# Optimization experiments

Hardware: AMD Instinct MI355X
Metric: run time of the kernel (lower is better)

## Reference

```python
import jax, jax.numpy as jnp
import numpy as np

IN_F = 4096
OUT_F = 4096
R_BLOCKS = 4
D = IN_F // R_BLOCKS          # 1024 block size
NUM_TASKS = 5
POOL = 5
EPS0 = 1e-05
SEQ = 4096


def setup_inputs() -> dict:
    key = jax.random.key(0)
    k1, k2, k3, k4 = jax.random.split(key, 4)
    return {
        "input": jax.random.normal(k1, (1, SEQ, IN_F), jnp.float32),
        "lora_route": jax.random.normal(k2, (NUM_TASKS, IN_F, POOL), jnp.float32) * 0.02,
        "lora_down": jax.random.normal(k3, (NUM_TASKS, R_BLOCKS, D, D), jnp.float32) * 0.01,
        "W": jax.random.normal(k4, (OUT_F, IN_F), jnp.float32) * 0.02,
        "task_id": 5,
    }


def _block_diag(Q):
    # Q: [r, d, d] -> [r*d, r*d] block-diagonal
    r, d, _ = Q.shape
    out = jnp.zeros((r * d, r * d), Q.dtype)
    for i in range(r):
        out = out.at[i * d:(i + 1) * d, i * d:(i + 1) * d].set(Q[i])
    return out


def reference(input, lora_route, lora_down, W, task_id):
    # eval-mode forward of OFTInjectedLinear (block_share=False, is_coft=True)
    n_tasks, in_f, pool = lora_route.shape
    r, d = lora_down.shape[1], lora_down.shape[2]
    # project_batch: eps = (eps0 * d * d) / sqrt(r)
    eps = jnp.asarray(EPS0 * d * d, input.dtype) / jnp.sqrt(jnp.asarray(r, input.dtype))

    route = lora_route[task_id - 1][None]                     # [1, in, pool]
    input_mean = jnp.mean(input, axis=1, keepdims=True)       # [1, 1, in]
    omegas = jax.nn.softmax(jnp.matmul(input_mean, route), axis=2)  # [1, 1, pool]
    omegas_mean = jnp.mean(omegas, axis=(0, 1))[:task_id]     # [task_id]
    k = min(task_id, 2)
    _, I_idx = jax.lax.top_k(omegas_mean, k)                  # selected tasks

    eye_d = jnp.eye(d, dtype=input.dtype)
    delta = jnp.eye(in_f, dtype=input.dtype)
    for i in range(k):                                        # k is a small static int
        j = I_idx[i]
        R = jnp.take(lora_down, j, axis=0)                    # [r, d, d]
        # COFT projection toward the ZERO matrix (source uses torch.zeros for I)
        nrm = jnp.sqrt(jnp.sum(R * R, axis=(1, 2), keepdims=True))  # per-block fro norm
        Rp = jnp.where(nrm <= eps, R, eps * R / jnp.maximum(nrm, 1e-12))
        # batched Cayley: Q = (I - skew) (I + skew)^{-1}
        skew = 0.5 * (Rp - jnp.swapaxes(Rp, 1, 2))
        Q = jnp.matmul(eye_d - skew, jnp.linalg.inv(eye_d + skew))  # [r, d, d]
        bd = _block_diag(Q)                                   # [in, in]
        omega_j = omegas[0, 0, j]                             # scalar (B==1)
        delta = delta * (omega_j * bd)                        # ELEMENTWISE, as in source

    filt = jnp.matmul(delta, W.T)                             # [in, out]
    return jnp.matmul(input, filt)                            # [1, S, out]
```

## Files before the change

kernel.cpp:

```cpp
#include <hip/hip_runtime.h>
#include <stdint.h>


typedef __bf16 bf16;
typedef __bf16 bf16x4 __attribute__((ext_vector_type(4)));
typedef __bf16 bf16x8 __attribute__((ext_vector_type(8)));
typedef float  f32x4  __attribute__((ext_vector_type(4)));

#define AS1 __attribute__((address_space(1)))
#define AS3 __attribute__((address_space(3)))

constexpr size_t OFF_INBF = 0;
constexpr size_t OFF_WV   = OFF_INBF + (size_t)4096 * 4096 * 2;
constexpr size_t OFF_MEAN = OFF_WV + (size_t)4096 * 4096 * 2;
constexpr size_t OFF_INFO = OFF_MEAN + 4096 * 4;
constexpr size_t OFF_V    = OFF_INFO + 64;
constexpr size_t TP_ELEMS  = (size_t)16 * 8192;
constexpr size_t OFF_MPART = OFF_WV + (size_t)1024 * 1024;

__global__ void mean_cvt(const float4* __restrict__ in4, float* __restrict__ mpart,
                         bf16* __restrict__ ob) {
    const int t  = threadIdx.x;
    const int f4 = blockIdx.x * 256 + t;
    const int by = blockIdx.y;
    const int s0 = by * 32;
    float sx = 0.f, sy = 0.f, sz = 0.f, sw = 0.f;
    for (int s = s0; s < s0 + 32; ++s) {
        float4 vx = in4[(size_t)s * 1024 + f4];
        sx += vx.x; sy += vx.y; sz += vx.z; sw += vx.w;
        bf16x4 bv;
        bv[0] = (bf16)vx.x; bv[1] = (bf16)vx.y; bv[2] = (bf16)vx.z; bv[3] = (bf16)vx.w;
        *(bf16x4*)&ob[(size_t)s * 4096 + f4 * 4] = bv;
    }
    float4* mp = (float4*)&mpart[(size_t)by * 4096 + f4 * 4];
    *mp = make_float4(sx, sy, sz, sw);
}

__global__ void omega_kernel(const float* __restrict__ mpart, const float* __restrict__ lora_route,
                             const int* __restrict__ task_id_p, int* __restrict__ info_i,
                             float* __restrict__ info_f) {
    __shared__ float wpart[16][5];
    const int t = threadIdx.x;
    const int tid = task_id_p[0];
    const float* route = lora_route + (size_t)(tid - 1) * 4096 * 5;
    float acc[5] = {0.f, 0.f, 0.f, 0.f, 0.f};
#pragma unroll
    for (int ff = 0; ff < 4; ++ff) {
        const int f = ff * 1024 + t;
        float cs = 0.f;
        for (int by = 0; by < 128; ++by) cs += mpart[(size_t)by * 4096 + f];
        const float m = cs * (1.0f / 4096.0f);
#pragma unroll
        for (int p = 0; p < 5; ++p) acc[p] += m * route[f * 5 + p];
    }
#pragma unroll
    for (int p = 0; p < 5; ++p)
        for (int off = 32; off > 0; off >>= 1) acc[p] += __shfl_xor(acc[p], off);
    if ((t & 63) == 0) {
#pragma unroll
        for (int p = 0; p < 5; ++p) wpart[t >> 6][p] = acc[p];
    }
    __syncthreads();
    if (t == 0) {
        float logits[5];
        for (int p = 0; p < 5; ++p) {
            float s = 0.f;
            for (int ww = 0; ww < 16; ++ww) s += wpart[ww][p];
            logits[p] = s;
        }
        float mx = logits[0];
        for (int p = 1; p < 5; ++p) mx = fmaxf(mx, logits[p]);
        float e[5], se = 0.f;
        for (int p = 0; p < 5; ++p) { e[p] = expf(logits[p] - mx); se += e[p]; }
        float om[5];
        for (int p = 0; p < 5; ++p) om[p] = e[p] / se;
        const int n = tid < 5 ? tid : 5;
        int j1 = 0;
        for (int p = 1; p < n; ++p) if (om[p] > om[j1]) j1 = p;
        int j2 = -1;
        for (int p = 0; p < n; ++p) if (p != j1 && (j2 < 0 || om[p] > om[j2])) j2 = p;
        const int k = tid < 2 ? tid : 2;
        info_i[0] = j1;
        info_i[1] = (k > 1) ? j2 : j1;
        info_i[2] = k;
        float c = om[j1];
        if (k > 1) c *= om[j2];
        info_f[3] = c;
    }
}

__global__ void diag_kernel(const float* __restrict__ lora_down, const int* __restrict__ info_i,
                            float* __restrict__ TP, float* __restrict__ NP) {
    const int bid = blockIdx.x;
    const int ts = bid >> 10;
    const int rb = (bid >> 8) & 3;
    const int a  = (bid >> 4) & 15;
    const int b  = bid & 15;
    const int k = info_i[2];
    if (ts >= k) return;
    const int j = info_i[ts];
    const float* R = lora_down + ((size_t)(j * 4 + rb) << 20);
    __shared__ float X[64][65];
    __shared__ float Y[64][65];
    __shared__ float wsum[4];
    const int t = threadIdx.x;
    const int i = t >> 2, g = t & 3;
    const int a64 = a * 64, b64 = b * 64;
    float nacc = 0.f;
#pragma unroll
    for (int qq = 0; qq < 4; ++qq) {
        const int fi = qq * 256 + t;
        const int row = fi >> 4, c4 = fi & 15;
        float4 vx = *(const float4*)&R[(size_t)(a64 + row) * 1024 + b64 + c4 * 4];
        X[row][c4 * 4 + 0] = vx.x; X[row][c4 * 4 + 1] = vx.y;
        X[row][c4 * 4 + 2] = vx.z; X[row][c4 * 4 + 3] = vx.w;
        nacc += vx.x * vx.x + vx.y * vx.y + vx.z * vx.z + vx.w * vx.w;
        float4 vy = *(const float4*)&R[(size_t)(b64 + row) * 1024 + a64 + c4 * 4];
        Y[row][c4 * 4 + 0] = vy.x; Y[row][c4 * 4 + 1] = vy.y;
        Y[row][c4 * 4 + 2] = vy.z; Y[row][c4 * 4 + 3] = vy.w;
    }
    __syncthreads();
    float tacc = 0.f;
#pragma unroll
    for (int s = 0; s < 16; ++s) {
        float d = X[i][g * 16 + s] - Y[g * 16 + s][i];
        tacc += d * d;
    }
    tacc += __shfl_xor(tacc, 1);
    tacc += __shfl_xor(tacc, 2);
    if (g == 0) TP[b * 8192 + ((ts * 4 + rb) << 10) + a64 + i] = tacc;
    for (int off = 32; off > 0; off >>= 1) nacc += __shfl_down(nacc, off);
    if ((t & 63) == 0) wsum[t >> 6] = nacc;
    __syncthreads();
    if (t == 0) NP[(ts * 4 + rb) * 256 + a * 16 + b] = wsum[0] + wsum[1] + wsum[2] + wsum[3];
}

__global__ void vbuild(const float* __restrict__ TP, const float* __restrict__ NP,
                       const int* __restrict__ info_i, const float* __restrict__ info_f,
                       float* __restrict__ v) {
    __shared__ float red[256];
    __shared__ float snrm[8];
    const int t = threadIdx.x;
    for (int g = 0; g < 8; ++g) {
        red[t] = NP[g * 256 + t];
        __syncthreads();
        for (int s = 128; s > 0; s >>= 1) {
            if (t < s) red[t] += red[t + s];
            __syncthreads();
        }
        if (t == 0) snrm[g] = red[0];
        __syncthreads();
    }
    const int i = blockIdx.x * 256 + t;
    const int k = info_i[2];
    const float c = info_f[3];
    const int rb = i >> 10, di = i & 1023;
    const float eps = 1e-5f * 1024.0f * 1024.0f / 2.0f;
    float q = c;
    for (int ts = 0; ts < k; ++ts) {
        float tt = 0.f;
#pragma unroll
        for (int bb = 0; bb < 16; ++bb) tt += TP[bb * 8192 + ((ts * 4 + rb) << 10) + di];
        float nrm = sqrtf(snrm[ts * 4 + rb]);
        float scale = (nrm <= eps) ? 1.0f : eps / fmaxf(nrm, 1e-12f);
        q *= 1.0f - 0.5f * scale * scale * tt;
    }
    v[i] = q;
}

__global__ void scaleW(const float4* __restrict__ W4, const float* __restrict__ v,
                       bf16* __restrict__ Wv) {
    const size_t stride = (size_t)gridDim.x * blockDim.x;
    for (size_t i = (size_t)blockIdx.x * blockDim.x + threadIdx.x; i < (size_t)4096 * 1024; i += stride) {
        float4 w = W4[i];
        const float* vp = &v[(i & 1023) << 2];
        bf16x4 o;
        o[0] = (bf16)(w.x * vp[0]);
        o[1] = (bf16)(w.y * vp[1]);
        o[2] = (bf16)(w.z * vp[2]);
        o[3] = (bf16)(w.w * vp[3]);
        *(bf16x4*)&Wv[i << 2] = o;
    }
}

__device__ __forceinline__ void gload_lds16(const bf16* g, bf16* lds) {
    __builtin_amdgcn_global_load_lds((const AS1 void*)g, (AS3 void*)lds, 16, 0, 0);
}

__global__ __launch_bounds__(512, 2) void gemm256(const bf16* __restrict__ A,
                                                  const bf16* __restrict__ B,
                                                  float* __restrict__ C) {
    __shared__ bf16 lds[65536];
    const int t = threadIdx.x;
    const int w = t >> 6, l = t & 63;
    const int bid = blockIdx.x;
    const int swz = ((bid & 7) << 5) | (bid >> 3);
    const int bm = swz >> 4, bn = swz & 15;
    const int wm = w >> 2, wn = w & 3;
    const int rl = l & 15, q = l >> 4;
    const int xm = (l & 7) << 4;

    const int srow = (w << 4) + (l >> 3);
    const int scol = ((l & 7) ^ (l >> 3)) << 3;
    const bf16* pA = A + (size_t)((bm << 8) + srow) * 4096 + scol;
    const bf16* pB = B + (size_t)((bn << 8) + srow) * 4096 + scol;

#define STG(dstE, srcP, h, kt) do {                                                          \
        gload_lds16((srcP) + (size_t)((h) * 128) * 4096 + (size_t)(kt) * 64,                 \
                    (bf16*)&lds[(dstE) + (h) * 8192 + w * 1024]);                            \
        gload_lds16((srcP) + (size_t)((h) * 128 + 8) * 4096 + (size_t)(kt) * 64,             \
                    (bf16*)&lds[(dstE) + (h) * 8192 + w * 1024 + 512]);                      \
    } while (0)

    const int aB = (((wm << 7) + rl) << 6);
    const int bB = 16384 + (((wn << 6) + rl) << 6);
    const int c0 = (((q << 4) + 0) ^ xm) >> 1;
    const int c1 = (((q << 4) + 64) ^ xm) >> 1;

    f32x4 acc[8][4] = {};
    bf16x8 a0L[4], a0H[4], a1L[4], a1H[4], b0[4], b1[4], a0n[4];

    STG(0, pA, 0, 0); STG(0, pA, 1, 0);
    STG(16384, pB, 0, 0); STG(16384, pB, 1, 0);
    STG(32768, pA, 0, 1); STG(32768, pA, 1, 1);
    asm volatile("s_waitcnt vmcnt(8)" ::: "memory");
    __builtin_amdgcn_s_barrier();
    asm volatile("" ::: "memory");
#pragma unroll
    for (int m = 0; m < 4; ++m) a0L[m] = *(const bf16x8*)&lds[0 + aB + m * 1024 + c0];

    for (int kt = 0; kt < 64; ++kt) {
        const int cur = (kt & 1) << 15;
        const int nxt = cur ^ 32768;
        if (kt < 63) asm volatile("s_waitcnt vmcnt(4)" ::: "memory");
        else         asm volatile("s_waitcnt vmcnt(0)" ::: "memory");
        __builtin_amdgcn_s_barrier();
        asm volatile("" ::: "memory");

#pragma unroll
        for (int n = 0; n < 4; ++n) b0[n] = *(const bf16x8*)&lds[cur + bB + n * 1024 + c0];
#pragma unroll
        for (int m = 0; m < 4; ++m) a0H[m] = *(const bf16x8*)&lds[cur + aB + (m + 4) * 1024 + c0];
        if (kt + 1 < 64) STG(nxt + 16384, pB, 0, kt + 1);
        __builtin_amdgcn_s_setprio(1);
#pragma unroll
        for (int m = 0; m < 4; ++m)
#pragma unroll
            for (int n = 0; n < 4; ++n)
                acc[m][n] = __builtin_amdgcn_mfma_f32_16x16x32_bf16(a0L[m], b0[n], acc[m][n], 0, 0, 0);
        __builtin_amdgcn_s_setprio(0);
        __builtin_amdgcn_s_barrier();

#pragma unroll
        for (int m = 0; m < 4; ++m) a1L[m] = *(const bf16x8*)&lds[cur + aB + m * 1024 + c1];
#pragma unroll
        for (int n = 0; n < 4; ++n) b1[n] = *(const bf16x8*)&lds[cur + bB + n * 1024 + c1];
        if (kt + 1 < 64) STG(nxt + 16384, pB, 1, kt + 1);
        __builtin_amdgcn_s_setprio(1);
#pragma unroll
        for (int m = 0; m < 4; ++m)
#pragma unroll
            for (int n = 0; n < 4; ++n)
                acc[m + 4][n] = __builtin_amdgcn_mfma_f32_16x16x32_bf16(a0H[m], b0[n], acc[m + 4][n], 0, 0, 0);
        __builtin_amdgcn_s_setprio(0);
        __builtin_amdgcn_s_barrier();

#pragma unroll
        for (int m = 0; m < 4; ++m) a1H[m] = *(const bf16x8*)&lds[cur + aB + (m + 4) * 1024 + c1];
        __builtin_amdgcn_s_setprio(1);
#pragma unroll
        for (int m = 0; m < 4; ++m)
#pragma unroll
            for (int n = 0; n < 4; ++n)
                acc[m][n] = __builtin_amdgcn_mfma_f32_16x16x32_bf16(a1L[m], b1[n], acc[m][n], 0, 0, 0);
        __builtin_amdgcn_s_setprio(0);
        asm volatile("s_waitcnt lgkmcnt(0)" ::: "memory");
        if (kt < 63) asm volatile("s_waitcnt vmcnt(4)" ::: "memory");
        __builtin_amdgcn_s_barrier();
        asm volatile("" ::: "memory");

        if (kt + 2 < 64) { STG(cur, pA, 0, kt + 2); STG(cur, pA, 1, kt + 2); }
        if (kt + 1 < 64) {
#pragma unroll
            for (int m = 0; m < 4; ++m) a0n[m] = *(const bf16x8*)&lds[nxt + aB + m * 1024 + c0];
        }
        __builtin_amdgcn_s_setprio(1);
#pragma unroll
        for (int m = 0; m < 4; ++m)
#pragma unroll
            for (int n = 0; n < 4; ++n)
                acc[m + 4][n] = __builtin_amdgcn_mfma_f32_16x16x32_bf16(a1H[m], b1[n], acc[m + 4][n], 0, 0, 0);
        __builtin_amdgcn_s_setprio(0);
        if (kt + 1 < 64) {
#pragma unroll
            for (int m = 0; m < 4; ++m) a0L[m] = a0n[m];
        }
    }
#undef STG

    const int crow = (bm << 8) + (wm << 7) + (q << 2);
    const int ccol = (bn << 8) + (wn << 6) + rl;
#pragma unroll
    for (int m = 0; m < 8; ++m)
#pragma unroll
        for (int n = 0; n < 4; ++n)
#pragma unroll
            for (int r = 0; r < 4; ++r)
                C[(size_t)(crow + m * 16 + r) * 4096 + ccol + n * 16] = acc[m][n][r];
}

extern "C" void kernel_launch(void* const* d_in, const int* in_sizes, int n_in,
                              void* d_out, int out_size, void* d_ws, size_t ws_size,
                              hipStream_t stream) {
    const float* input      = (const float*)d_in[0];
    const float* lora_route = (const float*)d_in[1];
    const float* lora_down  = (const float*)d_in[2];
    const float* W          = (const float*)d_in[3];
    const int*   task_id    = (const int*)d_in[4];

    char* ws = (char*)d_ws;
    bf16*  inbf    = (bf16*)(ws + OFF_INBF);
    bf16*  Wv      = (bf16*)(ws + OFF_WV);
    int*   info_i  = (int*)(ws + OFF_INFO);
    float* info_f  = (float*)(ws + OFF_INFO);
    float* v       = (float*)(ws + OFF_V);
    float* TP      = (float*)(ws + OFF_WV);
    float* NP      = TP + TP_ELEMS;
    float* mpart   = (float*)(ws + OFF_MPART);
    float* out     = (float*)d_out;

    mean_cvt<<<dim3(4, 128), 256, 0, stream>>>((const float4*)input, mpart, inbf);
    omega_kernel<<<1, 1024, 0, stream>>>(mpart, lora_route, task_id, info_i, info_f);
    diag_kernel<<<2048, 256, 0, stream>>>(lora_down, info_i, TP, NP);
    vbuild<<<16, 256, 0, stream>>>(TP, NP, info_i, info_f, v);
    scaleW<<<4096, 256, 0, stream>>>((const float4*)W, v, Wv);
    gemm256<<<256, 512, 0, stream>>>(inbf, Wv, out);
}
```

Before: 202.6 us.

## Restructure GEMM main loop into quadrant-based MFMA schedule with two-step unroll

Rewrites the bf16 GEMM main loop so each K-tile is processed as four 4x2 MFMA quadrants, each with both k-halves, instead of four 4x4 half-k phases. Global-to-LDS staging of A and B for upcoming tiles is interleaved between the quadrants, and the loop is unrolled by two with fixed cur/next buffers. The prologue now prefetches B for two tiles and A for one, and the barrier and lgkmcnt waits are reordered to fit. The aim is better overlap of LDS reads and global loads with MFMA work, at the cost of more barriers and more fragile ordering of the waits.

```diff
diff --git a/kernel.cpp b/kernel.cpp
--- a/kernel.cpp
+++ b/kernel.cpp
@@ -218,85 +218,95 @@
     const int c1 = (((q << 4) + 64) ^ xm) >> 1;
 
     f32x4 acc[8][4] = {};
-    bf16x8 a0L[4], a0H[4], a1L[4], a1H[4], b0[4], b1[4], a0n[4];
-
+    bf16x8 a03[4][2], a47[4][2], b01[2][2], b23[2][2];
+
+    STG(16384, pB, 0, 0); STG(16384, pB, 1, 0);
     STG(0, pA, 0, 0); STG(0, pA, 1, 0);
-    STG(16384, pB, 0, 0); STG(16384, pB, 1, 0);
-    STG(32768, pA, 0, 1); STG(32768, pA, 1, 1);
-    asm volatile("s_waitcnt vmcnt(8)" ::: "memory");
+    STG(32768 + 16384, pB, 0, 1); STG(32768 + 16384, pB, 1, 1);
+    asm volatile("s_waitcnt vmcnt(4)" ::: "memory");
     __builtin_amdgcn_s_barrier();
     asm volatile("" ::: "memory");
-#pragma unroll
-    for (int m = 0; m < 4; ++m) a0L[m] = *(const bf16x8*)&lds[0 + aB + m * 1024 + c0];
-
-    for (int kt = 0; kt < 64; ++kt) {
-        const int cur = (kt & 1) << 15;
-        const int nxt = cur ^ 32768;
-        if (kt < 63) asm volatile("s_waitcnt vmcnt(4)" ::: "memory");
+
+#define RD_A(dst, buf, mofs)                                                                  \
+    _Pragma("unroll") for (int mf = 0; mf < 4; ++mf) {                                        \
+        dst[mf][0] = *(const bf16x8*)&lds[(buf) + aB + (mf + (mofs)) * 1024 + c0];            \
+        dst[mf][1] = *(const bf16x8*)&lds[(buf) + aB + (mf + (mofs)) * 1024 + c1];            \
+    }
+#define RD_B(dst, buf, nofs)                                                                  \
+    _Pragma("unroll") for (int nf = 0; nf < 2; ++nf) {                                        \
+        dst[nf][0] = *(const bf16x8*)&lds[(buf) + bB + (nf + (nofs)) * 1024 + c0];            \
+        dst[nf][1] = *(const bf16x8*)&lds[(buf) + bB + (nf + (nofs)) * 1024 + c1];            \
+    }
+#define MFMA16(am, bn, mofs, nofs)                                                            \
+    __builtin_amdgcn_s_setprio(1);                                                            \
+    _Pragma("unroll") for (int mf = 0; mf < 4; ++mf)                                          \
+        _Pragma("unroll") for (int nf = 0; nf < 2; ++nf)                                      \
+            _Pragma("unroll") for (int ks = 0; ks < 2; ++ks)                                  \
+                acc[mf + (mofs)][nf + (nofs)] = __builtin_amdgcn_mfma_f32_16x16x32_bf16(      \
+                    am[mf][ks], bn[nf][ks], acc[mf + (mofs)][nf + (nofs)], 0, 0, 0);          \
+    __builtin_amdgcn_s_setprio(0);
+#define BAR() __builtin_amdgcn_s_barrier()
+#define LGKM0() asm volatile("s_waitcnt lgkmcnt(0)" ::: "memory")
+#define FENCE() asm volatile("" ::: "memory")
+
+    for (int it = 0; it < 32; ++it) {
+        const int kt = it << 1;
+        const int cur = 0, nxt = 32768;
+        RD_A(a03, cur, 0); RD_B(b01, cur, 0);
+        STG(nxt, pA, 0, kt + 1);
+        asm volatile("s_waitcnt lgkmcnt(8)" ::: "memory");
+        BAR(); LGKM0();
+        MFMA16(a03, b01, 0, 0);
+        BAR();
+        RD_B(b23, cur, 2);
+        STG(nxt, pA, 1, kt + 1);
+        FENCE();
+        BAR(); LGKM0();
+        MFMA16(a03, b23, 0, 2);
+        BAR();
+        RD_A(a47, cur, 4);
+        if (kt + 2 < 64) STG(cur + 16384, pB, 0, kt + 2);
+        FENCE();
+        BAR(); LGKM0();
+        MFMA16(a47, b23, 4, 2);
+        BAR();
+        if (kt + 2 < 64) STG(cur + 16384, pB, 1, kt + 2);
+        if (it < 31) asm volatile("s_waitcnt vmcnt(4)" ::: "memory");
         else         asm volatile("s_waitcnt vmcnt(0)" ::: "memory");
-        __builtin_amdgcn_s_barrier();
-        asm volatile("" ::: "memory");
-
-#pragma unroll
-        for (int n = 0; n < 4; ++n) b0[n] = *(const bf16x8*)&lds[cur + bB + n * 1024 + c0];
-#pragma unroll
-        for (int m = 0; m < 4; ++m) a0H[m] = *(const bf16x8*)&lds[cur + aB + (m + 4) * 1024 + c0];
-        if (kt + 1 < 64) STG(nxt + 16384, pB, 0, kt + 1);
-        __builtin_amdgcn_s_setprio(1);
-#pragma unroll
-        for (int m = 0; m < 4; ++m)
-#pragma unroll
-            for (int n = 0; n < 4; ++n)
-                acc[m][n] = __builtin_amdgcn_mfma_f32_16x16x32_bf16(a0L[m], b0[n], acc[m][n], 0, 0, 0);
-        __builtin_amdgcn_s_setprio(0);
-        __builtin_amdgcn_s_barrier();
-
-#pragma unroll
-        for (int m = 0; m < 4; ++m) a1L[m] = *(const bf16x8*)&lds[cur + aB + m * 1024 + c1];
-#pragma unroll
-        for (int n = 0; n < 4; ++n) b1[n] = *(const bf16x8*)&lds[cur + bB + n * 1024 + c1];
-        if (kt + 1 < 64) STG(nxt + 16384, pB, 1, kt + 1);
-        __builtin_amdgcn_s_setprio(1);
-#pragma unroll
-        for (int m = 0; m < 4; ++m)
-#pragma unroll
-            for (int n = 0; n < 4; ++n)
-                acc[m + 4][n] = __builtin_amdgcn_mfma_f32_16x16x32_bf16(a0H[m], b0[n], acc[m + 4][n], 0, 0, 0);
-        __builtin_amdgcn_s_setprio(0);
-        __builtin_amdgcn_s_barrier();
-
-#pragma unroll
-        for (int m = 0; m < 4; ++m) a1H[m] = *(const bf16x8*)&lds[cur + aB + (m + 4) * 1024 + c1];
-        __builtin_amdgcn_s_setprio(1);
-#pragma unroll
-        for (int m = 0; m < 4; ++m)
-#pragma unroll
-            for (int n = 0; n < 4; ++n)
-                acc[m][n] = __builtin_amdgcn_mfma_f32_16x16x32_bf16(a1L[m], b1[n], acc[m][n], 0, 0, 0);
-        __builtin_amdgcn_s_setprio(0);
-        asm volatile("s_waitcnt lgkmcnt(0)" ::: "memory");
-        if (kt < 63) asm volatile("s_waitcnt vmcnt(4)" ::: "memory");
-        __builtin_amdgcn_s_barrier();
-        asm volatile("" ::: "memory");
-
-        if (kt + 2 < 64) { STG(cur, pA, 0, kt + 2); STG(cur, pA, 1, kt + 2); }
-        if (kt + 1 < 64) {
-#pragma unroll
-            for (int m = 0; m < 4; ++m) a0n[m] = *(const bf16x8*)&lds[nxt + aB + m * 1024 + c0];
-        }
-        __builtin_amdgcn_s_setprio(1);
-#pragma unroll
-        for (int m = 0; m < 4; ++m)
-#pragma unroll
-            for (int n = 0; n < 4; ++n)
-                acc[m + 4][n] = __builtin_amdgcn_mfma_f32_16x16x32_bf16(a1H[m], b1[n], acc[m + 4][n], 0, 0, 0);
-        __builtin_amdgcn_s_setprio(0);
-        if (kt + 1 < 64) {
-#pragma unroll
-            for (int m = 0; m < 4; ++m) a0L[m] = a0n[m];
-        }
+        BAR(); FENCE();
+        MFMA16(a47, b01, 4, 0);
+        BAR();
+        RD_A(a03, nxt, 0); RD_B(b01, nxt, 0);
+        if (kt + 2 < 64) STG(cur, pA, 0, kt + 2);
+        asm volatile("s_waitcnt lgkmcnt(8)" ::: "memory");
+        BAR(); LGKM0();
+        MFMA16(a03, b01, 0, 0);
+        BAR();
+        RD_B(b23, nxt, 2);
+        if (kt + 2 < 64) STG(cur, pA, 1, kt + 2);
+        FENCE();
+        BAR(); LGKM0();
+        MFMA16(a03, b23, 0, 2);
+        BAR();
+        RD_A(a47, nxt, 4);
+        if (kt + 3 < 64) STG(nxt + 16384, pB, 0, kt + 3);
+        FENCE();
+        BAR(); LGKM0();
+        MFMA16(a47, b23, 4, 2);
+        BAR();
+        if (kt + 3 < 64) STG(nxt + 16384, pB, 1, kt + 3);
+        if (it < 31) asm volatile("s_waitcnt vmcnt(4)" ::: "memory");
+        BAR(); FENCE();
+        MFMA16(a47, b01, 4, 0);
+        BAR();
     }
 #undef STG
+#undef RD_A
+#undef RD_B
+#undef MFMA16
+#undef BAR
+#undef LGKM0
+#undef FENCE
 
     const int crow = (bm << 8) + (wm << 7) + (q << 2);
     const int ccol = (bn << 8) + (wn << 6) + rl;
```

After: 202.5 us. Within noise of the previous version (-0.1%).
